# Optimization experiments

Measured on AMD Instinct MI355X. Metric: run time of the kernel, lower is better.

## Reference

```python
import jax, jax.numpy as jnp
import numpy as np

V = 50257; E = 1024; H = 1024; L = 256; NL = 2; D = 10


def setup_inputs() -> dict:
    key = jax.random.key(0)
    ks = jax.random.split(key, 16)
    n = lambda k, s: jax.random.normal(k, s, dtype=jnp.float32)
    return {
        "input_tok": jax.random.randint(ks[0], (1, 1), 0, V),
        "h0": n(ks[1], (NL, 1, H)),
        "c0": n(ks[2], (NL, 1, H)),
        "h_s": n(ks[3], (L, 1, H)),
        "h_t_tilde": n(ks[4], (1, 1, H)),
        "emb": n(ks[5], (V, E)) * 0.02,
        "Wp": n(ks[6], (H, H)) * (H ** -0.5),
        "wdot": n(ks[7], (1, H)) * (H ** -0.5),
        "Wbil": n(ks[8], (1, H, H)) * (H ** -0.5),
        "Wcomb": n(ks[9], (H, 2 * H)) * ((2 * H) ** -0.5),
        "bcomb": jnp.zeros((H,), jnp.float32),
        "Wih0": n(ks[10], (4 * H, E + H)) * ((E + H) ** -0.5),
        "Whh0": n(ks[11], (4 * H, H)) * (H ** -0.5),
        "bih0": jnp.zeros((4 * H,), jnp.float32),
        "bhh0": jnp.zeros((4 * H,), jnp.float32),
        "Wih1": n(ks[12], (4 * H, H)) * (H ** -0.5),
        "Whh1": n(ks[13], (4 * H, H)) * (H ** -0.5),
        "bih1": jnp.zeros((4 * H,), jnp.float32),
        "bhh1": jnp.zeros((4 * H,), jnp.float32),
        "Wout": n(ks[14], (V, H)) * (H ** -0.5),
        "bout": jnp.zeros((V,), jnp.float32),
    }


def _lstm_cell(x, h, c, Wih, Whh, bih, bhh):
    # torch LSTM gate order: i, f, g, o
    g = x @ Wih.T + bih + h @ Whh.T + bhh
    i, f, gg, o = jnp.split(g, 4, axis=-1)
    c2 = jax.nn.sigmoid(f) * c + jax.nn.sigmoid(i) * jnp.tanh(gg)
    h2 = jax.nn.sigmoid(o) * jnp.tanh(c2)
    return h2, c2


def reference(input_tok, h0, c0, h_s, h_t_tilde, emb, Wp, wdot, Wbil, Wcomb, bcomb,
              Wih0, Whh0, bih0, bhh0, Wih1, Whh1, bih1, bhh1, Wout, bout):
    embedding = emb[input_tok]                                  # [1,1,E]
    x = jnp.concatenate((embedding, h_t_tilde), axis=-1)[0]     # [1,E+H]
    h1, c1 = _lstm_cell(x, h0[0], c0[0], Wih0, Whh0, bih0, bhh0)
    h2, c2 = _lstm_cell(h1, h0[1], c0[1], Wih1, Whh1, bih1, bhh1)
    h_new = jnp.stack((h1, h2)); c_new = jnp.stack((c1, c2))
    h_t = h2                                                    # [1,H]
    Ls = h_s.shape[0]
    p_t = Ls * jax.nn.sigmoid(jnp.tanh(h_t @ Wp.T) @ wdot.T).squeeze()  # scalar
    s = jnp.round(p_t).astype(jnp.int32)
    idx = jnp.arange(Ls)
    lo = jnp.maximum(s - D, 0); hi = jnp.minimum(s + D, Ls - 1)
    mask = (idx >= lo) & (idx <= hi)                            # [L] local window
    # bilinear score h_t^T W h_s over all positions; mask outside window
    score = jnp.einsum('bh,ohk,lbk->lbo', h_t, Wbil, h_s)       # [L,1,1]
    neg = jnp.finfo(score.dtype).min
    a = jax.nn.softmax(jnp.where(mask[:, None, None], score, neg), axis=0)
    # NOTE: original uses exp(+d^2/(D/2)^2) (no minus sign); replicated faithfully.
    expo = jnp.where(mask, ((idx.astype(jnp.float32) - p_t) ** 2) / ((D / 2) ** 2), 0.0)
    a_t = a * jnp.exp(expo)[:, None, None]                      # [L,1,1]
    win = (hi - lo + 1).astype(jnp.float32)
    context = jnp.sum(a_t * h_s, axis=0, keepdims=True) / win   # [1,1,H] (mean over window)
    cat = jnp.concatenate((context, h_t[None]), axis=-1)        # [1,1,2H]
    h_t_tilde_new = jnp.tanh(cat @ Wcomb.T + bcomb)             # [1,1,H]
    y = jax.nn.log_softmax(h_t_tilde_new @ Wout.T + bout, axis=-1)  # [1,1,V]
    return (y, h_new, c_new, h_t_tilde_new, a_t, p_t)
```

## Files before the change

### kernel.cpp

```cpp
#include <hip/hip_runtime.h>
#include <math.h>

#define V 50257
#define E 1024
#define HH 1024
#define LL 256

#define O_H  (V)
#define O_C  (V + 2*HH)
#define O_HT (V + 4*HH)
#define O_A  (V + 5*HH)
#define O_P  (V + 5*HH + LL)

#define W_T    0
#define W_V    1024
#define W_SC   2048
#define W_CTX  2304
#define W_Z    4096
#define W_BM   54400
#define W_BS   55424

#define NB_LOGITS 786

__device__ __forceinline__ float sigmoidf_(float x) { return 1.f / (1.f + expf(-x)); }
__device__ __forceinline__ float dot4(float4 a, float4 b) {
    return a.x * b.x + a.y * b.y + a.z * b.z + a.w * b.w;
}

__device__ __forceinline__ float block_sum(float v, float* red) {
    int lane = threadIdx.x & 63, wv = threadIdx.x >> 6;
#pragma unroll
    for (int o = 32; o > 0; o >>= 1) v += __shfl_down(v, o, 64);
    if (lane == 0) red[wv] = v;
    __syncthreads();
    return red[0] + red[1] + red[2] + red[3];
}

__global__ void k_lstm(const float* __restrict__ Wih, const float* __restrict__ Whh,
                       const float* __restrict__ bih, const float* __restrict__ bhh,
                       const float* __restrict__ xa_base, const int* __restrict__ tok,
                       const float* __restrict__ xb, int na, int nb,
                       const float* __restrict__ hprev, const float* __restrict__ cprev,
                       float* __restrict__ hout, float* __restrict__ cout,
                       float* __restrict__ zero_buf) {
    const int u = blockIdx.x;
    const int K = na + nb;
    const int K4 = K >> 2, na4 = na >> 2;
    if (zero_buf && threadIdx.x == 0) zero_buf[u] = 0.f;
    const float* xa = tok ? (xa_base + (size_t)tok[0] * na) : xa_base;
    const float4* xa4 = (const float4*)xa;
    const float4* xb4 = (const float4*)xb;
    const float4* r0 = (const float4*)(Wih + (size_t)u * K);
    const float4* r1 = (const float4*)(Wih + (size_t)(u + HH) * K);
    const float4* r2 = (const float4*)(Wih + (size_t)(u + 2*HH) * K);
    const float4* r3 = (const float4*)(Wih + (size_t)(u + 3*HH) * K);
    float a0 = 0, a1 = 0, a2 = 0, a3 = 0;
    for (int j = threadIdx.x; j < K4; j += 256) {
        float4 xv = (j < na4) ? xa4[j] : xb4[j - na4];
        a0 += dot4(r0[j], xv); a1 += dot4(r1[j], xv);
        a2 += dot4(r2[j], xv); a3 += dot4(r3[j], xv);
    }
    const float4* s0 = (const float4*)(Whh + (size_t)u * HH);
    const float4* s1 = (const float4*)(Whh + (size_t)(u + HH) * HH);
    const float4* s2 = (const float4*)(Whh + (size_t)(u + 2*HH) * HH);
    const float4* s3 = (const float4*)(Whh + (size_t)(u + 3*HH) * HH);
    const float4* hp4 = (const float4*)hprev;
    {
        int j = threadIdx.x;
        float4 hv = hp4[j];
        a0 += dot4(s0[j], hv); a1 += dot4(s1[j], hv);
        a2 += dot4(s2[j], hv); a3 += dot4(s3[j], hv);
    }
    int lane = threadIdx.x & 63, wv = threadIdx.x >> 6;
#pragma unroll
    for (int o = 32; o > 0; o >>= 1) {
        a0 += __shfl_down(a0, o, 64);
        a1 += __shfl_down(a1, o, 64);
        a2 += __shfl_down(a2, o, 64);
        a3 += __shfl_down(a3, o, 64);
    }
    __shared__ float sm[4][4];
    if (lane == 0) { sm[wv][0] = a0; sm[wv][1] = a1; sm[wv][2] = a2; sm[wv][3] = a3; }
    __syncthreads();
    if (threadIdx.x == 0) {
        float gi = sm[0][0]+sm[1][0]+sm[2][0]+sm[3][0] + bih[u]        + bhh[u];
        float gf = sm[0][1]+sm[1][1]+sm[2][1]+sm[3][1] + bih[u+HH]     + bhh[u+HH];
        float gg = sm[0][2]+sm[1][2]+sm[2][2]+sm[3][2] + bih[u+2*HH]   + bhh[u+2*HH];
        float go = sm[0][3]+sm[1][3]+sm[2][3]+sm[3][3] + bih[u+3*HH]   + bhh[u+3*HH];
        float c = sigmoidf_(gf) * cprev[u] + sigmoidf_(gi) * tanhf(gg);
        hout[u] = sigmoidf_(go) * tanhf(c);
        cout[u] = c;
    }
}

__global__ void k_ptv(const float* __restrict__ Wp, const float* __restrict__ Wbil,
                      const float* __restrict__ h2, float* __restrict__ t_out,
                      float* __restrict__ v_out) {
    __shared__ float red[4];
    if (blockIdx.x < HH) {
        int r = blockIdx.x;
        const float4* row = (const float4*)(Wp + (size_t)r * HH);
        const float4* h24 = (const float4*)h2;
        float acc = dot4(row[threadIdx.x], h24[threadIdx.x]);
        float tot = block_sum(acc, red);
        if (threadIdx.x == 0) t_out[r] = tanhf(tot);
    } else {
        int b = blockIdx.x - HH;
        int h0 = b * 32;
        int k4 = threadIdx.x;
        const float4* W4 = (const float4*)Wbil;
        float4 acc = make_float4(0.f, 0.f, 0.f, 0.f);
        for (int h = h0; h < h0 + 32; ++h) {
            float hv = h2[h];
            float4 w = W4[(size_t)h * 256 + k4];
            acc.x += hv * w.x; acc.y += hv * w.y;
            acc.z += hv * w.z; acc.w += hv * w.w;
        }
        atomicAdd(&v_out[k4 * 4 + 0], acc.x);
        atomicAdd(&v_out[k4 * 4 + 1], acc.y);
        atomicAdd(&v_out[k4 * 4 + 2], acc.z);
        atomicAdd(&v_out[k4 * 4 + 3], acc.w);
    }
}

__global__ void k_score_p(const float* __restrict__ wdot, const float* __restrict__ t,
                          const float* __restrict__ v, const float* __restrict__ hs,
                          float* __restrict__ score, float* __restrict__ pt) {
    __shared__ float red[4];
    if (blockIdx.x == 0) {
        const float4* w4 = (const float4*)wdot;
        const float4* t4 = (const float4*)t;
        float acc = dot4(w4[threadIdx.x], t4[threadIdx.x]);
        float tot = block_sum(acc, red);
        if (threadIdx.x == 0) pt[0] = (float)LL * sigmoidf_(tot);
    } else {
        int l = blockIdx.x - 1;
        const float4* row = (const float4*)(hs + (size_t)l * HH);
        const float4* v4  = (const float4*)v;
        float acc = dot4(row[threadIdx.x], v4[threadIdx.x]);
        float tot = block_sum(acc, red);
        if (threadIdx.x == 0) score[l] = tot;
    }
}

__global__ void k_ctx(const float* __restrict__ score, const float* __restrict__ pt,
                      const float* __restrict__ hs, float* __restrict__ ctx,
                      float* __restrict__ a_out) {
    int l = threadIdx.x;
    float p = pt[0];
    int si = (int)rintf(p);
    int lo = max(si - 10, 0), hi = min(si + 10, LL - 1);
    bool mask = (l >= lo) && (l <= hi);
    float sc = score[l];
    __shared__ float sm[256];
    __shared__ float sa[256];
    sm[l] = mask ? sc : -INFINITY;
    __syncthreads();
    for (int s = 128; s > 0; s >>= 1) { if (l < s) sm[l] = fmaxf(sm[l], sm[l + s]); __syncthreads(); }
    float M = sm[0];
    __syncthreads();
    float e = mask ? expf(sc - M) : 0.f;
    sm[l] = e;
    __syncthreads();
    for (int s = 128; s > 0; s >>= 1) { if (l < s) sm[l] += sm[l + s]; __syncthreads(); }
    float S = sm[0];
    float d = (float)l - p;
    sa[l] = mask ? (e / S) * expf(d * d * 0.04f) : 0.f;
    __syncthreads();
    if (blockIdx.x == 4) {
        a_out[l] = sa[l];
    } else {
        int h = blockIdx.x * 256 + l;
        float acc = 0.f;
        for (int ll = lo; ll <= hi; ++ll)
            acc += sa[ll] * hs[(size_t)ll * HH + h];
        ctx[h] = acc;
    }
}

__global__ void k_comb(const float* __restrict__ Wcomb, const float* __restrict__ bcomb,
                       const float* __restrict__ ctx, const float* __restrict__ h2,
                       const float* __restrict__ pt, float* __restrict__ outv) {
    __shared__ float red[4];
    int u = blockIdx.x;
    float p = pt[0];
    int si = (int)rintf(p);
    int lo = max(si - 10, 0), hi = min(si + 10, LL - 1);
    float inv_win = 1.f / (float)(hi - lo + 1);
    const float4* row  = (const float4*)(Wcomb + (size_t)u * (2 * HH));
    const float4* ctx4 = (const float4*)ctx;
    const float4* h24  = (const float4*)h2;
    float acc = 0;
#pragma unroll
    for (int j = threadIdx.x; j < 512; j += 256) {
        float4 xv;
        if (j < 256) {
            xv = ctx4[j];
            xv.x *= inv_win; xv.y *= inv_win; xv.z *= inv_win; xv.w *= inv_win;
        } else {
            xv = h24[j - 256];
        }
        acc += dot4(row[j], xv);
    }
    float tot = block_sum(acc, red);
    if (threadIdx.x == 0) outv[u] = tanhf(tot + bcomb[u]);
}

__global__ void k_logits(const float* __restrict__ Wout, const float* __restrict__ bout,
                         const float* __restrict__ x, float* __restrict__ z,
                         float* __restrict__ bmax, float* __restrict__ bsum) {
    __shared__ float4 sx[256];
    sx[threadIdx.x] = ((const float4*)x)[threadIdx.x];
    __syncthreads();
    int lane = threadIdx.x & 63, wv = threadIdx.x >> 6;
    int base = blockIdx.x * 64 + wv * 16;
    float m = -INFINITY, s = 0.f;
    for (int t = 0; t < 16; ++t) {
        int r = base + t;
        if (r >= V) break;
        const float4* row = (const float4*)(Wout + (size_t)r * 1024);
        float acc = 0;
#pragma unroll
        for (int j = 0; j < 4; ++j)
            acc += dot4(row[lane + 64 * j], sx[lane + 64 * j]);
#pragma unroll
        for (int o = 32; o > 0; o >>= 1) acc += __shfl_xor(acc, o, 64);
        float zz = acc + bout[r];
        if (lane == 0) z[r] = zz;
        if (zz > m) { s *= expf(m - zz); m = zz; }
        s += expf(zz - m);
    }
    __shared__ float wm[4], wsv[4];
    if (lane == 0) { wm[wv] = m; wsv[wv] = s; }
    __syncthreads();
    if (threadIdx.x == 0) {
        float M = fmaxf(fmaxf(wm[0], wm[1]), fmaxf(wm[2], wm[3]));
        float S = 0.f;
        if (M != -INFINITY) {
#pragma unroll
            for (int w = 0; w < 4; ++w)
                if (wm[w] != -INFINITY) S += wsv[w] * expf(wm[w] - M);
        }
        bmax[blockIdx.x] = M; bsum[blockIdx.x] = S;
    }
}

__global__ void k_sub(const float* __restrict__ z, const float* __restrict__ bmax,
                      const float* __restrict__ bsum, int n, float* __restrict__ y) {
    int tid = threadIdx.x;
    float m = -INFINITY, s = 0.f;
    for (int i = tid; i < n; i += 256) {
        float m2 = bmax[i], s2 = bsum[i];
        float M = fmaxf(m, m2);
        if (M != -INFINITY) s = s * expf(m - M) + s2 * expf(m2 - M);
        m = M;
    }
    int lane = tid & 63, wv = tid >> 6;
#pragma unroll
    for (int o = 32; o > 0; o >>= 1) {
        float m2 = __shfl_down(m, o, 64), s2 = __shfl_down(s, o, 64);
        float M = fmaxf(m, m2);
        if (M != -INFINITY) s = s * expf(m - M) + s2 * expf(m2 - M);
        else s = 0.f;
        m = M;
    }
    __shared__ float wm[4], wsv[4];
    __shared__ float lzs;
    if (lane == 0) { wm[wv] = m; wsv[wv] = s; }
    __syncthreads();
    if (tid == 0) {
        float M = -INFINITY, S = 0.f;
#pragma unroll
        for (int w = 0; w < 4; ++w) {
            float M2 = fmaxf(M, wm[w]);
            if (M2 != -INFINITY) S = S * expf(M - M2) + wsv[w] * expf(wm[w] - M2);
            M = M2;
        }
        lzs = M + logf(S);
    }
    __syncthreads();
    float lz = lzs;
    int i = blockIdx.x * 256 + tid;
    if (i < V) y[i] = z[i] - lz;
}

extern "C" void kernel_launch(void* const* d_in, const int* in_sizes, int n_in,
                              void* d_out, int out_size, void* d_ws, size_t ws_size,
                              hipStream_t stream) {
    const int*   tok   = (const int*)  d_in[0];
    const float* h0    = (const float*)d_in[1];
    const float* c0    = (const float*)d_in[2];
    const float* hs    = (const float*)d_in[3];
    const float* htt   = (const float*)d_in[4];
    const float* emb   = (const float*)d_in[5];
    const float* Wp    = (const float*)d_in[6];
    const float* wdot  = (const float*)d_in[7];
    const float* Wbil  = (const float*)d_in[8];
    const float* Wcomb = (const float*)d_in[9];
    const float* bcomb = (const float*)d_in[10];
    const float* Wih0  = (const float*)d_in[11];
    const float* Whh0  = (const float*)d_in[12];
    const float* bih0  = (const float*)d_in[13];
    const float* bhh0  = (const float*)d_in[14];
    const float* Wih1  = (const float*)d_in[15];
    const float* Whh1  = (const float*)d_in[16];
    const float* bih1  = (const float*)d_in[17];
    const float* bhh1  = (const float*)d_in[18];
    const float* Wout  = (const float*)d_in[19];
    const float* bout  = (const float*)d_in[20];

    float* out = (float*)d_out;
    float* ws  = (float*)d_ws;

    float* h1o  = out + O_H;
    float* h2o  = out + O_H + HH;
    float* c1o  = out + O_C;
    float* c2o  = out + O_C + HH;
    float* htto = out + O_HT;
    float* ato  = out + O_A;
    float* pto  = out + O_P;

    hipLaunchKernelGGL(k_lstm, dim3(1024), dim3(256), 0, stream,
                       Wih0, Whh0, bih0, bhh0, emb, tok, htt, 1024, 1024,
                       h0, c0, h1o, c1o, ws + W_V);
    hipLaunchKernelGGL(k_lstm, dim3(1024), dim3(256), 0, stream,
                       Wih1, Whh1, bih1, bhh1, h1o, (const int*)nullptr, h1o, 1024, 0,
                       h0 + HH, c0 + HH, h2o, c2o, (float*)nullptr);
    hipLaunchKernelGGL(k_ptv, dim3(1024 + 32), dim3(256), 0, stream,
                       Wp, Wbil, h2o, ws + W_T, ws + W_V);
    hipLaunchKernelGGL(k_score_p, dim3(257), dim3(256), 0, stream,
                       wdot, ws + W_T, ws + W_V, hs, ws + W_SC, pto);
    hipLaunchKernelGGL(k_ctx, dim3(5), dim3(256), 0, stream,
                       ws + W_SC, pto, hs, ws + W_CTX, ato);
    hipLaunchKernelGGL(k_comb, dim3(1024), dim3(256), 0, stream,
                       Wcomb, bcomb, ws + W_CTX, h2o, pto, htto);
    hipLaunchKernelGGL(k_logits, dim3(NB_LOGITS), dim3(256), 0, stream,
                       Wout, bout, htto, ws + W_Z, ws + W_BM, ws + W_BS);
    hipLaunchKernelGGL(k_sub, dim3((V + 255) / 256), dim3(256), 0, stream,
                       ws + W_Z, ws + W_BM, ws + W_BS, NB_LOGITS, out);
}
```

Baseline: 91.27 us.

## Fuse attention into one window-only kernel and logits+logsoftmax via cooperative grid sync

Merges the score and context kernels into a single-block attention kernel that computes p_t first and scores only the rows inside the local window instead of all 256 rows. It also fuses the logits pass and the log-softmax subtraction into one cooperative kernel that uses a grid-wide sync in place of a separate launch. The intent is to drop two launches and skip unused score work. The cost is that the attention work now runs serially in one block, and the cooperative launch needs all 786 blocks resident at the same time.

After: 188.2 us. 106% more time.

```diff
diff --git a/kernel.cpp b/kernel.cpp
--- a/kernel.cpp
+++ b/kernel.cpp
@@ -1,5 +1,8 @@
 #include <hip/hip_runtime.h>
+#include <hip/hip_cooperative_groups.h>
 #include <math.h>
+
+namespace cg = cooperative_groups;
 
 #define V 50257
 #define E 1024
@@ -14,7 +17,6 @@
 
 #define W_T    0
 #define W_V    1024
-#define W_SC   2048
 #define W_CTX  2304
 #define W_Z    4096
 #define W_BM   54400
@@ -123,59 +125,61 @@
     }
 }
 
-__global__ void k_score_p(const float* __restrict__ wdot, const float* __restrict__ t,
-                          const float* __restrict__ v, const float* __restrict__ hs,
-                          float* __restrict__ score, float* __restrict__ pt) {
+__global__ void k_attn(const float* __restrict__ wdot, const float* __restrict__ t,
+                       const float* __restrict__ v, const float* __restrict__ hs,
+                       float* __restrict__ ctx, float* __restrict__ a_out,
+                       float* __restrict__ pt_out) {
+    const int tid = threadIdx.x;
+    const int lane = tid & 63, wv = tid >> 6;
     __shared__ float red[4];
-    if (blockIdx.x == 0) {
+    __shared__ float s_p;
+    __shared__ float ssc[32];
+    __shared__ float sa[LL];
+    {
         const float4* w4 = (const float4*)wdot;
         const float4* t4 = (const float4*)t;
-        float acc = dot4(w4[threadIdx.x], t4[threadIdx.x]);
+        float acc = dot4(w4[tid], t4[tid]);
         float tot = block_sum(acc, red);
-        if (threadIdx.x == 0) pt[0] = (float)LL * sigmoidf_(tot);
-    } else {
-        int l = blockIdx.x - 1;
+        if (tid == 0) { s_p = (float)LL * sigmoidf_(tot); pt_out[0] = s_p; }
+    }
+    __syncthreads();
+    const float p = s_p;
+    const int si = (int)rintf(p);
+    const int lo = max(si - 10, 0), hi = min(si + 10, LL - 1);
+    const int W = hi - lo + 1;
+    const float4* v4 = (const float4*)v;
+    for (int l = lo + wv; l <= hi; l += 4) {
         const float4* row = (const float4*)(hs + (size_t)l * HH);
-        const float4* v4  = (const float4*)v;
-        float acc = dot4(row[threadIdx.x], v4[threadIdx.x]);
-        float tot = block_sum(acc, red);
-        if (threadIdx.x == 0) score[l] = tot;
-    }
-}
-
-__global__ void k_ctx(const float* __restrict__ score, const float* __restrict__ pt,
-                      const float* __restrict__ hs, float* __restrict__ ctx,
-                      float* __restrict__ a_out) {
-    int l = threadIdx.x;
-    float p = pt[0];
-    int si = (int)rintf(p);
-    int lo = max(si - 10, 0), hi = min(si + 10, LL - 1);
-    bool mask = (l >= lo) && (l <= hi);
-    float sc = score[l];
-    __shared__ float sm[256];
-    __shared__ float sa[256];
-    sm[l] = mask ? sc : -INFINITY;
-    __syncthreads();
-    for (int s = 128; s > 0; s >>= 1) { if (l < s) sm[l] = fmaxf(sm[l], sm[l + s]); __syncthreads(); }
-    float M = sm[0];
-    __syncthreads();
-    float e = mask ? expf(sc - M) : 0.f;
-    sm[l] = e;
-    __syncthreads();
-    for (int s = 128; s > 0; s >>= 1) { if (l < s) sm[l] += sm[l + s]; __syncthreads(); }
-    float S = sm[0];
-    float d = (float)l - p;
-    sa[l] = mask ? (e / S) * expf(d * d * 0.04f) : 0.f;
-    __syncthreads();
-    if (blockIdx.x == 4) {
-        a_out[l] = sa[l];
-    } else {
-        int h = blockIdx.x * 256 + l;
-        float acc = 0.f;
-        for (int ll = lo; ll <= hi; ++ll)
-            acc += sa[ll] * hs[(size_t)ll * HH + h];
-        ctx[h] = acc;
-    }
+        float a = 0.f;
+#pragma unroll
+        for (int j = lane; j < 256; j += 64) a += dot4(row[j], v4[j]);
+#pragma unroll
+        for (int o = 32; o > 0; o >>= 1) a += __shfl_xor(a, o, 64);
+        if (lane == 0) ssc[l - lo] = a;
+    }
+    __syncthreads();
+    float M = -INFINITY;
+    for (int i = 0; i < W; ++i) M = fmaxf(M, ssc[i]);
+    float S = 0.f;
+    for (int i = 0; i < W; ++i) S += expf(ssc[i] - M);
+    {
+        bool mask = (tid >= lo) && (tid <= hi);
+        int wi = min(max(tid - lo, 0), 31);
+        float e = mask ? expf(ssc[wi] - M) : 0.f;
+        float d = (float)tid - p;
+        float at = mask ? (e / S) * expf(d * d * 0.04f) : 0.f;
+        sa[tid] = at;
+        a_out[tid] = at;
+    }
+    __syncthreads();
+    const float4* hs4 = (const float4*)hs;
+    float4 c = make_float4(0.f, 0.f, 0.f, 0.f);
+    for (int l = lo; l <= hi; ++l) {
+        float a = sa[l];
+        float4 hv = hs4[(size_t)l * 256 + tid];
+        c.x += a * hv.x; c.y += a * hv.y; c.z += a * hv.z; c.w += a * hv.w;
+    }
+    ((float4*)ctx)[tid] = c;
 }
 
 __global__ void k_comb(const float* __restrict__ Wcomb, const float* __restrict__ bcomb,
@@ -206,31 +210,49 @@
     if (threadIdx.x == 0) outv[u] = tanhf(tot + bcomb[u]);
 }
 
-__global__ void k_logits(const float* __restrict__ Wout, const float* __restrict__ bout,
-                         const float* __restrict__ x, float* __restrict__ z,
-                         float* __restrict__ bmax, float* __restrict__ bsum) {
+__global__ void k_logits_fused(const float* __restrict__ Wout, const float* __restrict__ bout,
+                               const float* __restrict__ x, float* __restrict__ z,
+                               float* __restrict__ bmax, float* __restrict__ bsum,
+                               float* __restrict__ y) {
     __shared__ float4 sx[256];
     sx[threadIdx.x] = ((const float4*)x)[threadIdx.x];
     __syncthreads();
-    int lane = threadIdx.x & 63, wv = threadIdx.x >> 6;
-    int base = blockIdx.x * 64 + wv * 16;
+    const int lane = threadIdx.x & 63, wv = threadIdx.x >> 6;
+    const int base = blockIdx.x * 64 + wv * 16;
     float m = -INFINITY, s = 0.f;
-    for (int t = 0; t < 16; ++t) {
-        int r = base + t;
-        if (r >= V) break;
-        const float4* row = (const float4*)(Wout + (size_t)r * 1024);
-        float acc = 0;
-#pragma unroll
-        for (int j = 0; j < 4; ++j)
-            acc += dot4(row[lane + 64 * j], sx[lane + 64 * j]);
-#pragma unroll
-        for (int o = 32; o > 0; o >>= 1) acc += __shfl_xor(acc, o, 64);
-        float zz = acc + bout[r];
-        if (lane == 0) z[r] = zz;
-        if (zz > m) { s *= expf(m - zz); m = zz; }
-        s += expf(zz - m);
+    if (base + 16 <= V) {
+#pragma unroll 4
+        for (int t = 0; t < 16; ++t) {
+            const int r = base + t;
+            const float4* row = (const float4*)(Wout + (size_t)r * 1024);
+            float acc = 0.f;
+#pragma unroll
+            for (int j = 0; j < 4; ++j) acc += dot4(row[lane + 64*j], sx[lane + 64*j]);
+#pragma unroll
+            for (int o = 32; o > 0; o >>= 1) acc += __shfl_xor(acc, o, 64);
+            float zz = acc + bout[r];
+            if (lane == 0) z[r] = zz;
+            if (zz > m) { s *= expf(m - zz); m = zz; }
+            s += expf(zz - m);
+        }
+    } else {
+        for (int t = 0; t < 16; ++t) {
+            const int r = base + t;
+            if (r >= V) break;
+            const float4* row = (const float4*)(Wout + (size_t)r * 1024);
+            float acc = 0.f;
+#pragma unroll
+            for (int j = 0; j < 4; ++j) acc += dot4(row[lane + 64*j], sx[lane + 64*j]);
+#pragma unroll
+            for (int o = 32; o > 0; o >>= 1) acc += __shfl_xor(acc, o, 64);
+            float zz = acc + bout[r];
+            if (lane == 0) z[r] = zz;
+            if (zz > m) { s *= expf(m - zz); m = zz; }
+            s += expf(zz - m);
+        }
     }
     __shared__ float wm[4], wsv[4];
+    __shared__ float lzs;
     if (lane == 0) { wm[wv] = m; wsv[wv] = s; }
     __syncthreads();
     if (threadIdx.x == 0) {
@@ -243,32 +265,26 @@
         }
         bmax[blockIdx.x] = M; bsum[blockIdx.x] = S;
     }
-}
-
-__global__ void k_sub(const float* __restrict__ z, const float* __restrict__ bmax,
-                      const float* __restrict__ bsum, int n, float* __restrict__ y) {
-    int tid = threadIdx.x;
-    float m = -INFINITY, s = 0.f;
-    for (int i = tid; i < n; i += 256) {
+    cg::this_grid().sync();
+    float mm = -INFINITY, ss = 0.f;
+    for (int i = threadIdx.x; i < NB_LOGITS; i += 256) {
         float m2 = bmax[i], s2 = bsum[i];
-        float M = fmaxf(m, m2);
-        if (M != -INFINITY) s = s * expf(m - M) + s2 * expf(m2 - M);
-        m = M;
-    }
-    int lane = tid & 63, wv = tid >> 6;
+        float M = fmaxf(mm, m2);
+        if (M != -INFINITY) ss = ss * expf(mm - M) + s2 * expf(m2 - M);
+        mm = M;
+    }
 #pragma unroll
     for (int o = 32; o > 0; o >>= 1) {
-        float m2 = __shfl_down(m, o, 64), s2 = __shfl_down(s, o, 64);
-        float M = fmaxf(m, m2);
-        if (M != -INFINITY) s = s * expf(m - M) + s2 * expf(m2 - M);
-        else s = 0.f;
-        m = M;
-    }
-    __shared__ float wm[4], wsv[4];
-    __shared__ float lzs;
-    if (lane == 0) { wm[wv] = m; wsv[wv] = s; }
-    __syncthreads();
-    if (tid == 0) {
+        float m2 = __shfl_down(mm, o, 64), s2 = __shfl_down(ss, o, 64);
+        float M = fmaxf(mm, m2);
+        if (M != -INFINITY) ss = ss * expf(mm - M) + s2 * expf(m2 - M);
+        else ss = 0.f;
+        mm = M;
+    }
+    __syncthreads();
+    if (lane == 0) { wm[wv] = mm; wsv[wv] = ss; }
+    __syncthreads();
+    if (threadIdx.x == 0) {
         float M = -INFINITY, S = 0.f;
 #pragma unroll
         for (int w = 0; w < 4; ++w) {
@@ -279,9 +295,9 @@
         lzs = M + logf(S);
     }
     __syncthreads();
-    float lz = lzs;
-    int i = blockIdx.x * 256 + tid;
-    if (i < V) y[i] = z[i] - lz;
+    const float lz = lzs;
+    int r = blockIdx.x * 64 + threadIdx.x;
+    if (threadIdx.x < 64 && r < V) y[r] = z[r] - lz;
 }
 
 extern "C" void kernel_launch(void* const* d_in, const int* in_sizes, int n_in,
@@ -328,14 +344,19 @@
                        h0 + HH, c0 + HH, h2o, c2o, (float*)nullptr);
     hipLaunchKernelGGL(k_ptv, dim3(1024 + 32), dim3(256), 0, stream,
                        Wp, Wbil, h2o, ws + W_T, ws + W_V);
-    hipLaunchKernelGGL(k_score_p, dim3(257), dim3(256), 0, stream,
-                       wdot, ws + W_T, ws + W_V, hs, ws + W_SC, pto);
-    hipLaunchKernelGGL(k_ctx, dim3(5), dim3(256), 0, stream,
-                       ws + W_SC, pto, hs, ws + W_CTX, ato);
+    hipLaunchKernelGGL(k_attn, dim3(1), dim3(256), 0, stream,
+                       wdot, ws + W_T, ws + W_V, hs, ws + W_CTX, ato, pto);
     hipLaunchKernelGGL(k_comb, dim3(1024), dim3(256), 0, stream,
                        Wcomb, bcomb, ws + W_CTX, h2o, pto, htto);
-    hipLaunchKernelGGL(k_logits, dim3(NB_LOGITS), dim3(256), 0, stream,
-                       Wout, bout, htto, ws + W_Z, ws + W_BM, ws + W_BS);
-    hipLaunchKernelGGL(k_sub, dim3((V + 255) / 256), dim3(256), 0, stream,
-                       ws + W_Z, ws + W_BM, ws + W_BS, NB_LOGITS, out);
-}
+    {
+        const float* xx = htto;
+        float* zp  = ws + W_Z;
+        float* bmp = ws + W_BM;
+        float* bsp = ws + W_BS;
+        float* yp  = out;
+        void* args[] = {(void*)&Wout, (void*)&bout, (void*)&xx,
+                        (void*)&zp, (void*)&bmp, (void*)&bsp, (void*)&yp};
+        hipLaunchCooperativeKernel((const void*)k_logits_fused, dim3(NB_LOGITS), dim3(256),
+                                   args, 0, stream);
+    }
+}
```
